# Optimization experiments

Measured on AMD Instinct MI355X. Metric: run time of the kernel, lower is better.

Reference implementation:

```python
import jax, jax.numpy as jnp
import numpy as np
from jax import lax

EPS = 1e-5


def _bn(x, gamma, beta, mean, var):
    # x: [B,C,H,W]; params: [C]
    inv = gamma / jnp.sqrt(var + EPS)
    return x * inv[None, :, None, None] + (beta - mean * inv)[None, :, None, None]


def _conv1x1(x, w):
    # w: [O, C] pointwise conv
    return jnp.einsum('oc,bchw->bohw', w, x)


def setup_inputs() -> dict:
    dim, num_heads = 256, 8
    B, H, W = 4, 40, 40
    key = jax.random.key(0)
    ks = jax.random.split(key, 12)
    inp = {
        'x': jax.random.normal(ks[0], (B, dim, H, W), jnp.float32),
        # qkv: Conv(dim, 2*dim, k=1) = conv1x1 (no bias) + BN + SiLU
        'qkv_w': jax.random.normal(ks[1], (2 * dim, dim), jnp.float32) * 0.05,
        'qkv_gamma': jax.random.uniform(ks[2], (2 * dim,), jnp.float32, 0.5, 1.5),
        'qkv_beta': jax.random.normal(ks[3], (2 * dim,), jnp.float32) * 0.05,
        'qkv_mean': jax.random.normal(ks[4], (2 * dim,), jnp.float32) * 0.05,
        'qkv_var': jax.random.uniform(ks[5], (2 * dim,), jnp.float32, 0.5, 1.5),
        # proj: Conv(dim, dim, k=1)
        'proj_w': jax.random.normal(ks[6], (dim, dim), jnp.float32) * 0.05,
        'proj_gamma': jax.random.uniform(ks[7], (dim,), jnp.float32, 0.5, 1.5),
        'proj_beta': jax.random.normal(ks[8], (dim,), jnp.float32) * 0.05,
        'proj_mean': jax.random.normal(ks[9], (dim,), jnp.float32) * 0.05,
        'proj_var': jax.random.uniform(ks[10], (dim,), jnp.float32, 0.5, 1.5),
        # pe: depthwise 3x3 conv (groups=dim, no bias) + BN (no activation)
        'pe_w': jax.random.normal(ks[11], (dim, 1, 3, 3), jnp.float32) * 0.1,
        'pe_gamma': jax.random.uniform(jax.random.fold_in(key, 100), (dim,), jnp.float32, 0.5, 1.5),
        'pe_beta': jax.random.normal(jax.random.fold_in(key, 101), (dim,), jnp.float32) * 0.05,
        'pe_mean': jax.random.normal(jax.random.fold_in(key, 102), (dim,), jnp.float32) * 0.05,
        'pe_var': jax.random.uniform(jax.random.fold_in(key, 103), (dim,), jnp.float32, 0.5, 1.5),
    }
    return inp


def reference(x, qkv_w, qkv_gamma, qkv_beta, qkv_mean, qkv_var,
              proj_w, proj_gamma, proj_beta, proj_mean, proj_var,
              pe_w, pe_gamma, pe_beta, pe_mean, pe_var):
    B, C, H, W = x.shape
    num_heads = 8
    head_dim = C // num_heads
    N = H * W

    # positional encoding: depthwise 3x3 conv + BN
    pe = lax.conv_general_dilated(
        x, pe_w, window_strides=(1, 1), padding='SAME',
        feature_group_count=C, dimension_numbers=('NCHW', 'OIHW', 'NCHW'))
    pe = _bn(pe, pe_gamma, pe_beta, pe_mean, pe_var)

    # qkv: 1x1 conv + BN + SiLU, then split into q, k along channels
    qkv = jax.nn.silu(_bn(_conv1x1(x, qkv_w), qkv_gamma, qkv_beta, qkv_mean, qkv_var))
    q, k = qkv[:, :C], qkv[:, C:]
    v = x + pe

    # reshape to heads: q,v -> [B,h,N,d]; k -> [B,h,d,N]
    q = q.reshape(B, num_heads, head_dim, N).transpose(0, 1, 3, 2)
    k = k.reshape(B, num_heads, head_dim, N)
    v = v.reshape(B, num_heads, head_dim, N).transpose(0, 1, 3, 2)

    scale = head_dim ** (-0.5)
    attn = jnp.einsum('bhnd,bhdm->bhnm', q, k) * scale  # [B,h,N,N]
    attn = jax.nn.softmax(attn, axis=-1)
    out = jnp.einsum('bhnm,bhmd->bhnd', attn, v)        # [B,h,N,d]
    out = out.transpose(0, 1, 3, 2).reshape(B, C, H, W)

    # proj: 1x1 conv + BN + SiLU
    return jax.nn.silu(_bn(_conv1x1(out, proj_w), proj_gamma, proj_beta, proj_mean, proj_var))
```

## Files before the change

kernel.cpp:

```cpp
#include <hip/hip_runtime.h>
#include <hip/hip_bf16.h>

typedef __attribute__((ext_vector_type(8))) short short8;
typedef __attribute__((ext_vector_type(4))) float f32x4;

__device__ __forceinline__ unsigned short f2bf(float f){
    union { float f; unsigned u; } uf; uf.f = f;
    unsigned u = uf.u;
    u += 0x7FFFu + ((u >> 16) & 1u);
    return (unsigned short)(u >> 16);
}
__device__ __forceinline__ int pack2(float a, float b){
    union { float f; unsigned u; } ua, ub; ua.f = a; ub.f = b;
    unsigned x = ua.u; x += 0x7FFFu + ((x >> 16) & 1u);
    unsigned y = ub.u; y += 0x7FFFu + ((y >> 16) & 1u);
    return (int)((x >> 16) | (y & 0xFFFF0000u));
}
__device__ __forceinline__ unsigned cvtpk(float lo, float hi){
    unsigned r;
    asm("v_cvt_pk_bf16_f32 %0, %1, %2" : "=v"(r) : "v"(lo), "v"(hi));
    return r;
}
__device__ __forceinline__ float fexp2(float x){
    return __builtin_amdgcn_exp2f(x);
}
__device__ __forceinline__ void load_lds16(const void* g, void* l){
    __builtin_amdgcn_global_load_lds(
        (const __attribute__((address_space(1))) unsigned int*)g,
        (__attribute__((address_space(3))) unsigned int*)l,
        16, 0, 0);
}

#define N_SPATIAL 1600
#define QSCALE_LOG2E 0.25506601f
#define LSTR 40

__global__ __launch_bounds__(256) void k_head(const float* __restrict__ x,
                                              const float* __restrict__ pw,
                                              const float* __restrict__ pg,
                                              const float* __restrict__ pb,
                                              const float* __restrict__ pm,
                                              const float* __restrict__ pv,
                                              unsigned short* __restrict__ x_t,
                                              unsigned short* __restrict__ v_mf){
    __shared__ float xs[32][163];
    int bi = blockIdx.x;
    int t = threadIdx.x;
    if (bi < 200){
        int b = bi / 50, nc = bi % 50;
        int n0 = nc * 32;
        int c = t;
        unsigned short vals[32];
        const float* src = x + ((size_t)(b*256 + c))*N_SPATIAL + n0;
        #pragma unroll
        for (int j=0;j<8;j++){
            float4 f = *reinterpret_cast<const float4*>(src + j*4);
            vals[j*4+0] = f2bf(f.x); vals[j*4+1] = f2bf(f.y);
            vals[j*4+2] = f2bf(f.z); vals[j*4+3] = f2bf(f.w);
        }
        unsigned short* dst = x_t + ((size_t)b*N_SPATIAL + n0)*256 + c;
        #pragma unroll
        for (int j=0;j<32;j++) dst[(size_t)j*256] = vals[j];
        return;
    }
    int pbi = bi - 200;
    int b = pbi/200, h=(pbi/25)%8, kt=pbi%25;
    int winStart = kt*64 - 48;
    const float* xbase = x + ((size_t)(b*256 + h*32))*N_SPATIAL;
    #pragma unroll
    for (int i=0;i<20;i++){
        int idx = t + i*256;
        int row = idx / 160, col = idx - row*160;
        int n = winStart + col;
        float val = ((unsigned)n < 1600u) ? xbase[(size_t)row*N_SPATIAL + n] : 0.f;
        xs[row][col] = val;
    }
    __syncthreads();

    int f = t>>6, lane = t&63, ql = lane&15, lg = lane>>4;
    int d = (f>>1)*16 + ql;
    int c = h*32 + d;
    float inv = pg[c]*rsqrtf(pv[c]+1e-5f);
    float bias = pb[c]-pm[c]*inv;
    const float* w9 = pw + c*9;
    float w00=w9[0],w01=w9[1],w02=w9[2],w10=w9[3],w11=w9[4],w12=w9[5],w20=w9[6],w21=w9[7],w22=w9[8];
    const float* xr = xs[d];
    union { unsigned short u[8]; int4 i4; } vals;
    #pragma unroll
    for (int j=0;j<8;j++){
        int key = (f&1)*32 + (j>>2)*16 + 4*lg + (j&3);
        int n = kt*64 + key;
        int hh = n/40, ww = n - hh*40;
        int col = key + 48;
        float acc = 0.f;
        if (hh > 0){
            if (ww > 0)  acc += xr[col-41]*w00;
                         acc += xr[col-40]*w01;
            if (ww < 39) acc += xr[col-39]*w02;
        }
        if (ww > 0)  acc += xr[col-1]*w10;
                     acc += xr[col]*w11;
        if (ww < 39) acc += xr[col+1]*w12;
        if (hh < 39){
            if (ww > 0)  acc += xr[col+39]*w20;
                         acc += xr[col+40]*w21;
            if (ww < 39) acc += xr[col+41]*w22;
        }
        float out = xr[col] + acc*inv + bias;
        vals.u[j] = f2bf(out);
    }
    *reinterpret_cast<int4*>(v_mf + ((size_t)(pbi*4 + f)*64 + lane)*8) = vals.i4;
}

__global__ __launch_bounds__(256) void k_qkv2(const unsigned short* __restrict__ x_t,
                                              const float* __restrict__ wq,
                                              const float* __restrict__ g,
                                              const float* __restrict__ be,
                                              const float* __restrict__ mu,
                                              const float* __restrict__ va,
                                              unsigned short* __restrict__ q_t,
                                              unsigned short* __restrict__ k_mf){
    __shared__ alignas(16) unsigned short a_lds[64*LSTR];
    __shared__ alignas(16) unsigned short b_lds[64*LSTR];
    int bi = blockIdx.x;
    int b = bi / 200, ot = (bi/25) % 8, nt = bi % 25;
    int o0 = ot*64, n0 = nt*64;
    int tid = threadIdx.x, w = tid>>6, lane = tid&63;
    int row = tid>>2, col8 = (tid&3)*8;
    int ql = lane&15, lg = lane>>4;
    f32x4 acc[4];
    #pragma unroll
    for (int t=0;t<4;t++) acc[t] = (f32x4){0.f,0.f,0.f,0.f};
    const float* asrc = wq + (size_t)(o0+row)*256 + col8;
    const unsigned short* bsrc = x_t + ((size_t)b*N_SPATIAL + n0 + row)*256 + col8;
    for (int k0=0; k0<256; k0+=32){
        float4 f0 = *reinterpret_cast<const float4*>(asrc + k0);
        float4 f1 = *reinterpret_cast<const float4*>(asrc + k0 + 4);
        int4 av; av.x = pack2(f0.x,f0.y); av.y = pack2(f0.z,f0.w);
                 av.z = pack2(f1.x,f1.y); av.w = pack2(f1.z,f1.w);
        *reinterpret_cast<int4*>(&a_lds[row*LSTR + col8]) = av;
        *reinterpret_cast<int4*>(&b_lds[row*LSTR + col8]) = *reinterpret_cast<const int4*>(bsrc + k0);
        __syncthreads();
        short8 af = *reinterpret_cast<const short8*>(&a_lds[(16*w + ql)*LSTR + lg*8]);
        #pragma unroll
        for (int t=0;t<4;t++){
            short8 bf = *reinterpret_cast<const short8*>(&b_lds[(16*t + ql)*LSTR + lg*8]);
            acc[t] = __builtin_amdgcn_mfma_f32_16x16x32_bf16(af, bf, acc[t], 0, 0, 0);
        }
        __syncthreads();
    }
    int ob = o0 + 16*w + 4*lg;
    int d0 = ob & 31;
    float invr[4], b2r[4];
    #pragma unroll
    for (int r=0;r<4;r++){
        int o = ob + r;
        invr[r] = g[o] * rsqrtf(va[o] + 1e-5f);
        b2r[r]  = be[o] - mu[o]*invr[r];
    }
    if (ob < 256){
        int grp = ob >> 5;
        unsigned short* dstb = q_t + ((size_t)(b*8 + grp)*N_SPATIAL)*32 + d0;
        #pragma unroll
        for (int t=0;t<4;t++){
            int n = n0 + 16*t + ql;
            float y[4];
            #pragma unroll
            for (int r=0;r<4;r++){
                float z = acc[t][r]*invr[r] + b2r[r];
                y[r] = (z / (1.f + __expf(-z))) * QSCALE_LOG2E;
            }
            *reinterpret_cast<uint2*>(dstb + (size_t)n*32) =
                make_uint2((unsigned)pack2(y[0],y[1]), (unsigned)pack2(y[2],y[3]));
        }
    } else {
        int hh = (ob>>5) - 8;
        size_t kbase = (size_t)((b*8+hh)*25)*2048;
        #pragma unroll
        for (int t=0;t<4;t++){
            int n = n0 + 16*t + ql;
            int kt = n>>6, tf = (n>>4)&3, qr = n&15;
            float y[4];
            #pragma unroll
            for (int r=0;r<4;r++){
                float z = acc[t][r]*invr[r] + b2r[r];
                y[r] = z / (1.f + __expf(-z));
            }
            size_t off = kbase + (size_t)kt*2048 + tf*512 + ((d0>>3)*16 + qr)*8 + (d0&7);
            *reinterpret_cast<uint2*>(k_mf + off) =
                make_uint2((unsigned)pack2(y[0],y[1]), (unsigned)pack2(y[2],y[3]));
        }
    }
}

__global__ __launch_bounds__(256) void k_attn8(const unsigned short* __restrict__ q_t,
                                               const unsigned short* __restrict__ k_mf,
                                               const unsigned short* __restrict__ v_mf,
                                               unsigned short* __restrict__ ao_t){
    __shared__ alignas(16) unsigned short k_lds[4][2048];
    __shared__ alignas(16) unsigned short v_lds[4][2048];
    int l = blockIdx.x;
    int xc = l & 7, j = l >> 3;
    int gg = xc + 8*(j/25);
    int b = gg >> 3, h = gg & 7, qt = j % 25;
    int tid = threadIdx.x, w = tid>>6, lane = tid&63;
    int ql = lane&15, lg = lane>>4;
    int nq = qt*64 + w*16 + ql;

    const unsigned short* qsrc = q_t + ((size_t)(b*8+h)*N_SPATIAL)*32;
    const unsigned short* kms  = k_mf + (size_t)((b*8+h)*25)*2048;
    const unsigned short* vms  = v_mf + (size_t)(b*200 + h*25)*2048;

    short8 qf = *reinterpret_cast<const short8*>(qsrc + (size_t)nq*32 + lg*8);

    const unsigned short* kg = kms + w*512 + lane*8;
    const unsigned short* vg = vms + w*512 + lane*8;

    load_lds16(kg,        &k_lds[0][w*512]);
    load_lds16(vg,        &v_lds[0][w*512]);
    load_lds16(kg + 2048, &k_lds[1][w*512]);
    load_lds16(vg + 2048, &v_lds[1][w*512]);

    f32x4 o0 = (f32x4){0.f,0.f,0.f,0.f};
    f32x4 o1 = (f32x4){0.f,0.f,0.f,0.f};
    float Sp = 0.f;

    for (int kt = 0; kt < 25; ++kt){
        if (kt+2 < 25){
            int bidx = (kt+2)&3;
            load_lds16(kg + (size_t)(kt+2)*2048, &k_lds[bidx][w*512]);
            load_lds16(vg + (size_t)(kt+2)*2048, &v_lds[bidx][w*512]);
        }
        if (kt < 23)       asm volatile("s_waitcnt vmcnt(4)" ::: "memory");
        else if (kt == 23) asm volatile("s_waitcnt vmcnt(2)" ::: "memory");
        else               asm volatile("s_waitcnt vmcnt(0)" ::: "memory");
        __builtin_amdgcn_s_barrier();
        asm volatile("" ::: "memory");

        const unsigned short* kb = &k_lds[kt&3][0];
        const unsigned short* vb = &v_lds[kt&3][0];
        short8 ka0 = *reinterpret_cast<const short8*>(kb +    0 + lane*8);
        short8 ka1 = *reinterpret_cast<const short8*>(kb +  512 + lane*8);
        short8 ka2 = *reinterpret_cast<const short8*>(kb + 1024 + lane*8);
        short8 ka3 = *reinterpret_cast<const short8*>(kb + 1536 + lane*8);

        f32x4 z = (f32x4){0.f,0.f,0.f,0.f};
        f32x4 p0 = __builtin_amdgcn_mfma_f32_16x16x32_bf16(ka0, qf, z, 0,0,0);
        f32x4 p1 = __builtin_amdgcn_mfma_f32_16x16x32_bf16(ka1, qf, z, 0,0,0);
        f32x4 p2 = __builtin_amdgcn_mfma_f32_16x16x32_bf16(ka2, qf, z, 0,0,0);
        f32x4 p3 = __builtin_amdgcn_mfma_f32_16x16x32_bf16(ka3, qf, z, 0,0,0);

        #pragma unroll
        for (int r=0;r<4;r++){
            p0[r] = fexp2(p0[r]);
            p1[r] = fexp2(p1[r]);
            p2[r] = fexp2(p2[r]);
            p3[r] = fexp2(p3[r]);
        }
        Sp += ((p0[0]+p0[1])+(p0[2]+p0[3])) + ((p1[0]+p1[1])+(p1[2]+p1[3]))
            + ((p2[0]+p2[1])+(p2[2]+p2[3])) + ((p3[0]+p3[1])+(p3[2]+p3[3]));

        union { int4 i; short8 s8; } pb0, pb1;
        pb0.i = make_int4((int)cvtpk(p0[0],p0[1]), (int)cvtpk(p0[2],p0[3]),
                          (int)cvtpk(p1[0],p1[1]), (int)cvtpk(p1[2],p1[3]));
        pb1.i = make_int4((int)cvtpk(p2[0],p2[1]), (int)cvtpk(p2[2],p2[3]),
                          (int)cvtpk(p3[0],p3[1]), (int)cvtpk(p3[2],p3[3]));

        short8 va0 = *reinterpret_cast<const short8*>(vb +    0 + lane*8);
        short8 va1 = *reinterpret_cast<const short8*>(vb +  512 + lane*8);
        short8 va2 = *reinterpret_cast<const short8*>(vb + 1024 + lane*8);
        short8 va3 = *reinterpret_cast<const short8*>(vb + 1536 + lane*8);

        o0 = __builtin_amdgcn_mfma_f32_16x16x32_bf16(va0, pb0.s8, o0, 0,0,0);
        o0 = __builtin_amdgcn_mfma_f32_16x16x32_bf16(va1, pb1.s8, o0, 0,0,0);
        o1 = __builtin_amdgcn_mfma_f32_16x16x32_bf16(va2, pb0.s8, o1, 0,0,0);
        o1 = __builtin_amdgcn_mfma_f32_16x16x32_bf16(va3, pb1.s8, o1, 0,0,0);
    }

    Sp += __shfl_xor(Sp, 16);
    Sp += __shfl_xor(Sp, 32);
    float inv = 1.f / Sp;
    size_t rowoff = ((size_t)b*N_SPATIAL + nq)*256 + h*32;
    uint2 w0 = make_uint2((unsigned)pack2(o0[0]*inv, o0[1]*inv),
                          (unsigned)pack2(o0[2]*inv, o0[3]*inv));
    *reinterpret_cast<uint2*>(ao_t + rowoff + 4*lg) = w0;
    uint2 w1 = make_uint2((unsigned)pack2(o1[0]*inv, o1[1]*inv),
                          (unsigned)pack2(o1[2]*inv, o1[3]*inv));
    *reinterpret_cast<uint2*>(ao_t + rowoff + 16 + 4*lg) = w1;
}

__global__ __launch_bounds__(256) void k_proj2(const unsigned short* __restrict__ ao_t,
                                               const float* __restrict__ wp,
                                               const float* __restrict__ g,
                                               const float* __restrict__ be,
                                               const float* __restrict__ mu,
                                               const float* __restrict__ va,
                                               float* __restrict__ out){
    __shared__ alignas(16) unsigned short a_lds[64*LSTR];
    __shared__ alignas(16) unsigned short b_lds[64*LSTR];
    int bi = blockIdx.x;
    int b = bi / 100, ot = (bi/25) % 4, nt = bi % 25;
    int o0 = ot*64, n0 = nt*64;
    int tid = threadIdx.x, w = tid>>6, lane = tid&63;
    int row = tid>>2, col8 = (tid&3)*8;
    int ql = lane&15, lg = lane>>4;
    f32x4 acc[4];
    #pragma unroll
    for (int t=0;t<4;t++) acc[t] = (f32x4){0.f,0.f,0.f,0.f};
    const float* asrc = wp + (size_t)(o0+row)*256 + col8;
    const unsigned short* bsrc = ao_t + ((size_t)b*N_SPATIAL + n0 + row)*256 + col8;
    for (int k0=0; k0<256; k0+=32){
        float4 f0 = *reinterpret_cast<const float4*>(asrc + k0);
        float4 f1 = *reinterpret_cast<const float4*>(asrc + k0 + 4);
        int4 av; av.x = pack2(f0.x,f0.y); av.y = pack2(f0.z,f0.w);
                 av.z = pack2(f1.x,f1.y); av.w = pack2(f1.z,f1.w);
        *reinterpret_cast<int4*>(&a_lds[row*LSTR + col8]) = av;
        *reinterpret_cast<int4*>(&b_lds[row*LSTR + col8]) = *reinterpret_cast<const int4*>(bsrc + k0);
        __syncthreads();
        short8 af = *reinterpret_cast<const short8*>(&a_lds[(16*w + ql)*LSTR + lg*8]);
        #pragma unroll
        for (int t=0;t<4;t++){
            short8 bf = *reinterpret_cast<const short8*>(&b_lds[(16*t + ql)*LSTR + lg*8]);
            acc[t] = __builtin_amdgcn_mfma_f32_16x16x32_bf16(af, bf, acc[t], 0, 0, 0);
        }
        __syncthreads();
    }
    #pragma unroll
    for (int r=0;r<4;r++){
        int o = o0 + 16*w + lg*4 + r;
        float inv = g[o] * rsqrtf(va[o] + 1e-5f);
        float b2  = be[o] - mu[o]*inv;
        float* dst = out + ((size_t)(b*256 + o))*N_SPATIAL;
        #pragma unroll
        for (int t=0;t<4;t++){
            int n = n0 + 16*t + ql;
            float z = acc[t][r]*inv + b2;
            float y = z / (1.f + __expf(-z));
            dst[n] = y;
        }
    }
}

extern "C" void kernel_launch(void* const* d_in, const int* in_sizes, int n_in,
                              void* d_out, int out_size, void* d_ws, size_t ws_size,
                              hipStream_t stream) {
    const float* x      = (const float*)d_in[0];
    const float* qkv_w  = (const float*)d_in[1];
    const float* qkv_g  = (const float*)d_in[2];
    const float* qkv_b  = (const float*)d_in[3];
    const float* qkv_m  = (const float*)d_in[4];
    const float* qkv_v  = (const float*)d_in[5];
    const float* proj_w = (const float*)d_in[6];
    const float* proj_g = (const float*)d_in[7];
    const float* proj_b = (const float*)d_in[8];
    const float* proj_m = (const float*)d_in[9];
    const float* proj_v = (const float*)d_in[10];
    const float* pe_w   = (const float*)d_in[11];
    const float* pe_g   = (const float*)d_in[12];
    const float* pe_b   = (const float*)d_in[13];
    const float* pe_m   = (const float*)d_in[14];
    const float* pe_v   = (const float*)d_in[15];

    char* ws = (char*)d_ws;
    unsigned short* x_t  = (unsigned short*)(ws);
    unsigned short* v_mf = (unsigned short*)(ws + 3276800);
    unsigned short* q_t  = (unsigned short*)(ws + 6553600);
    unsigned short* k_mf = (unsigned short*)(ws + 9830400);
    unsigned short* ao_t = (unsigned short*)(ws + 13107200);
    float* outp = (float*)d_out;

    k_head <<<1000,256, 0, stream>>>(x, pe_w, pe_g, pe_b, pe_m, pe_v, x_t, v_mf);
    k_qkv2 <<<800, 256, 0, stream>>>(x_t, qkv_w, qkv_g, qkv_b, qkv_m, qkv_v, q_t, k_mf);
    k_attn8<<<800, 256, 0, stream>>>(q_t, k_mf, v_mf, ao_t);
    k_proj2<<<400, 256, 0, stream>>>(ao_t, proj_w, proj_g, proj_b, proj_m, proj_v, outp);
}
```

Before: 62.21 us.

## Split attention keys across two waves, fuse x transpose into head, shrink proj tiles

The attention kernel now uses 128-thread blocks. Each wave handles all 64 queries of a tile (four Q fragments) over half of the key tiles, double-buffering K and V into per-wave LDS. The two partial results and row sums are merged through LDS at the end. The x-to-bf16 transpose is folded into the depthwise-conv head blocks so they reuse x data already staged in LDS, removing 200 separate blocks. The projection GEMM uses 32-column tiles to double the grid to 800 blocks. The trade-offs are more registers per wave in attention, fewer waves per block, and an extra cross-wave combine step.

```diff
diff --git a/kernel.cpp b/kernel.cpp
--- a/kernel.cpp
+++ b/kernel.cpp
@@ -35,36 +35,18 @@
 #define QSCALE_LOG2E 0.25506601f
 #define LSTR 40
 
-__global__ __launch_bounds__(256) void k_head(const float* __restrict__ x,
-                                              const float* __restrict__ pw,
-                                              const float* __restrict__ pg,
-                                              const float* __restrict__ pb,
-                                              const float* __restrict__ pm,
-                                              const float* __restrict__ pv,
-                                              unsigned short* __restrict__ x_t,
-                                              unsigned short* __restrict__ v_mf){
+__global__ __launch_bounds__(256) void k_head2(const float* __restrict__ x,
+                                               const float* __restrict__ pw,
+                                               const float* __restrict__ pg,
+                                               const float* __restrict__ pb,
+                                               const float* __restrict__ pm,
+                                               const float* __restrict__ pv,
+                                               unsigned short* __restrict__ x_t,
+                                               unsigned short* __restrict__ v_mf){
     __shared__ float xs[32][163];
-    int bi = blockIdx.x;
+    int pbi = blockIdx.x;
+    int b = pbi/200, h=(pbi/25)%8, kt=pbi%25;
     int t = threadIdx.x;
-    if (bi < 200){
-        int b = bi / 50, nc = bi % 50;
-        int n0 = nc * 32;
-        int c = t;
-        unsigned short vals[32];
-        const float* src = x + ((size_t)(b*256 + c))*N_SPATIAL + n0;
-        #pragma unroll
-        for (int j=0;j<8;j++){
-            float4 f = *reinterpret_cast<const float4*>(src + j*4);
-            vals[j*4+0] = f2bf(f.x); vals[j*4+1] = f2bf(f.y);
-            vals[j*4+2] = f2bf(f.z); vals[j*4+3] = f2bf(f.w);
-        }
-        unsigned short* dst = x_t + ((size_t)b*N_SPATIAL + n0)*256 + c;
-        #pragma unroll
-        for (int j=0;j<32;j++) dst[(size_t)j*256] = vals[j];
-        return;
-    }
-    int pbi = bi - 200;
-    int b = pbi/200, h=(pbi/25)%8, kt=pbi%25;
     int winStart = kt*64 - 48;
     const float* xbase = x + ((size_t)(b*256 + h*32))*N_SPATIAL;
     #pragma unroll
@@ -76,6 +58,16 @@
         xs[row][col] = val;
     }
     __syncthreads();
+
+    {
+        unsigned short* xtb = x_t + ((size_t)b*N_SPATIAL + kt*64)*256 + h*32;
+        #pragma unroll
+        for (int i=0;i<8;i++){
+            int idx = t + i*256;
+            int cl = idx & 31, nl = idx >> 5;
+            xtb[(size_t)nl*256 + cl] = f2bf(xs[cl][nl + 48]);
+        }
+    }
 
     int f = t>>6, lane = t&63, ql = lane&15, lg = lane>>4;
     int d = (f>>1)*16 + ql;
@@ -193,103 +185,149 @@
     }
 }
 
-__global__ __launch_bounds__(256) void k_attn8(const unsigned short* __restrict__ q_t,
-                                               const unsigned short* __restrict__ k_mf,
-                                               const unsigned short* __restrict__ v_mf,
-                                               unsigned short* __restrict__ ao_t){
-    __shared__ alignas(16) unsigned short k_lds[4][2048];
-    __shared__ alignas(16) unsigned short v_lds[4][2048];
+__global__ __launch_bounds__(128) void k_attn10(const unsigned short* __restrict__ q_t,
+                                                const unsigned short* __restrict__ k_mf,
+                                                const unsigned short* __restrict__ v_mf,
+                                                unsigned short* __restrict__ ao_t){
+    __shared__ alignas(16) unsigned short lds_all[2][2][2][2048];
     int l = blockIdx.x;
     int xc = l & 7, j = l >> 3;
     int gg = xc + 8*(j/25);
     int b = gg >> 3, h = gg & 7, qt = j % 25;
     int tid = threadIdx.x, w = tid>>6, lane = tid&63;
     int ql = lane&15, lg = lane>>4;
-    int nq = qt*64 + w*16 + ql;
 
     const unsigned short* qsrc = q_t + ((size_t)(b*8+h)*N_SPATIAL)*32;
-    const unsigned short* kms  = k_mf + (size_t)((b*8+h)*25)*2048;
-    const unsigned short* vms  = v_mf + (size_t)(b*200 + h*25)*2048;
-
-    short8 qf = *reinterpret_cast<const short8*>(qsrc + (size_t)nq*32 + lg*8);
-
-    const unsigned short* kg = kms + w*512 + lane*8;
-    const unsigned short* vg = vms + w*512 + lane*8;
-
-    load_lds16(kg,        &k_lds[0][w*512]);
-    load_lds16(vg,        &v_lds[0][w*512]);
-    load_lds16(kg + 2048, &k_lds[1][w*512]);
-    load_lds16(vg + 2048, &v_lds[1][w*512]);
-
-    f32x4 o0 = (f32x4){0.f,0.f,0.f,0.f};
-    f32x4 o1 = (f32x4){0.f,0.f,0.f,0.f};
-    float Sp = 0.f;
-
-    for (int kt = 0; kt < 25; ++kt){
-        if (kt+2 < 25){
-            int bidx = (kt+2)&3;
-            load_lds16(kg + (size_t)(kt+2)*2048, &k_lds[bidx][w*512]);
-            load_lds16(vg + (size_t)(kt+2)*2048, &v_lds[bidx][w*512]);
-        }
-        if (kt < 23)       asm volatile("s_waitcnt vmcnt(4)" ::: "memory");
-        else if (kt == 23) asm volatile("s_waitcnt vmcnt(2)" ::: "memory");
-        else               asm volatile("s_waitcnt vmcnt(0)" ::: "memory");
-        __builtin_amdgcn_s_barrier();
-        asm volatile("" ::: "memory");
-
-        const unsigned short* kb = &k_lds[kt&3][0];
-        const unsigned short* vb = &v_lds[kt&3][0];
-        short8 ka0 = *reinterpret_cast<const short8*>(kb +    0 + lane*8);
-        short8 ka1 = *reinterpret_cast<const short8*>(kb +  512 + lane*8);
-        short8 ka2 = *reinterpret_cast<const short8*>(kb + 1024 + lane*8);
-        short8 ka3 = *reinterpret_cast<const short8*>(kb + 1536 + lane*8);
-
-        f32x4 z = (f32x4){0.f,0.f,0.f,0.f};
-        f32x4 p0 = __builtin_amdgcn_mfma_f32_16x16x32_bf16(ka0, qf, z, 0,0,0);
-        f32x4 p1 = __builtin_amdgcn_mfma_f32_16x16x32_bf16(ka1, qf, z, 0,0,0);
-        f32x4 p2 = __builtin_amdgcn_mfma_f32_16x16x32_bf16(ka2, qf, z, 0,0,0);
-        f32x4 p3 = __builtin_amdgcn_mfma_f32_16x16x32_bf16(ka3, qf, z, 0,0,0);
-
-        #pragma unroll
-        for (int r=0;r<4;r++){
-            p0[r] = fexp2(p0[r]);
-            p1[r] = fexp2(p1[r]);
-            p2[r] = fexp2(p2[r]);
-            p3[r] = fexp2(p3[r]);
-        }
-        Sp += ((p0[0]+p0[1])+(p0[2]+p0[3])) + ((p1[0]+p1[1])+(p1[2]+p1[3]))
-            + ((p2[0]+p2[1])+(p2[2]+p2[3])) + ((p3[0]+p3[1])+(p3[2]+p3[3]));
-
-        union { int4 i; short8 s8; } pb0, pb1;
-        pb0.i = make_int4((int)cvtpk(p0[0],p0[1]), (int)cvtpk(p0[2],p0[3]),
-                          (int)cvtpk(p1[0],p1[1]), (int)cvtpk(p1[2],p1[3]));
-        pb1.i = make_int4((int)cvtpk(p2[0],p2[1]), (int)cvtpk(p2[2],p2[3]),
-                          (int)cvtpk(p3[0],p3[1]), (int)cvtpk(p3[2],p3[3]));
-
-        short8 va0 = *reinterpret_cast<const short8*>(vb +    0 + lane*8);
-        short8 va1 = *reinterpret_cast<const short8*>(vb +  512 + lane*8);
-        short8 va2 = *reinterpret_cast<const short8*>(vb + 1024 + lane*8);
-        short8 va3 = *reinterpret_cast<const short8*>(vb + 1536 + lane*8);
-
-        o0 = __builtin_amdgcn_mfma_f32_16x16x32_bf16(va0, pb0.s8, o0, 0,0,0);
-        o0 = __builtin_amdgcn_mfma_f32_16x16x32_bf16(va1, pb1.s8, o0, 0,0,0);
-        o1 = __builtin_amdgcn_mfma_f32_16x16x32_bf16(va2, pb0.s8, o1, 0,0,0);
-        o1 = __builtin_amdgcn_mfma_f32_16x16x32_bf16(va3, pb1.s8, o1, 0,0,0);
-    }
-
-    Sp += __shfl_xor(Sp, 16);
-    Sp += __shfl_xor(Sp, 32);
-    float inv = 1.f / Sp;
-    size_t rowoff = ((size_t)b*N_SPATIAL + nq)*256 + h*32;
-    uint2 w0 = make_uint2((unsigned)pack2(o0[0]*inv, o0[1]*inv),
-                          (unsigned)pack2(o0[2]*inv, o0[3]*inv));
-    *reinterpret_cast<uint2*>(ao_t + rowoff + 4*lg) = w0;
-    uint2 w1 = make_uint2((unsigned)pack2(o1[0]*inv, o1[1]*inv),
-                          (unsigned)pack2(o1[2]*inv, o1[3]*inv));
-    *reinterpret_cast<uint2*>(ao_t + rowoff + 16 + 4*lg) = w1;
-}
-
-__global__ __launch_bounds__(256) void k_proj2(const unsigned short* __restrict__ ao_t,
+    const unsigned short* kms  = k_mf + (size_t)((b*8+h)*25)*2048 + lane*8;
+    const unsigned short* vms  = v_mf + (size_t)(b*200 + h*25)*2048 + lane*8;
+
+    short8 qf[4];
+    #pragma unroll
+    for (int qj=0;qj<4;qj++)
+        qf[qj] = *reinterpret_cast<const short8*>(qsrc + (size_t)(qt*64 + qj*16 + ql)*32 + lg*8);
+
+    f32x4 acc[2][4];
+    #pragma unroll
+    for (int di=0;di<2;di++)
+        #pragma unroll
+        for (int qj=0;qj<4;qj++) acc[di][qj] = (f32x4){0.f,0.f,0.f,0.f};
+    float Sp[4] = {0.f,0.f,0.f,0.f};
+
+    int t0 = w ? 13 : 0, t1 = w ? 25 : 13;
+    unsigned short* kb0 = &lds_all[w][0][0][0];
+    unsigned short* vb0 = &lds_all[w][0][1][0];
+    unsigned short* kb1 = &lds_all[w][1][0][0];
+    unsigned short* vb1 = &lds_all[w][1][1][0];
+
+    {
+        const unsigned short* ks = kms + (size_t)t0*2048;
+        const unsigned short* vs = vms + (size_t)t0*2048;
+        load_lds16(ks,        kb0);
+        load_lds16(ks +  512, kb0 +  512);
+        load_lds16(ks + 1024, kb0 + 1024);
+        load_lds16(ks + 1536, kb0 + 1536);
+        load_lds16(vs,        vb0);
+        load_lds16(vs +  512, vb0 +  512);
+        load_lds16(vs + 1024, vb0 + 1024);
+        load_lds16(vs + 1536, vb0 + 1536);
+    }
+
+    for (int i = t0; i < t1; ++i){
+        int cb = (i - t0) & 1;
+        unsigned short* kb = cb ? kb1 : kb0;
+        unsigned short* vb = cb ? vb1 : vb0;
+        if (i+1 < t1){
+            unsigned short* kn = cb ? kb0 : kb1;
+            unsigned short* vn = cb ? vb0 : vb1;
+            const unsigned short* ks = kms + (size_t)(i+1)*2048;
+            const unsigned short* vs = vms + (size_t)(i+1)*2048;
+            load_lds16(ks,        kn);
+            load_lds16(ks +  512, kn +  512);
+            load_lds16(ks + 1024, kn + 1024);
+            load_lds16(ks + 1536, kn + 1536);
+            load_lds16(vs,        vn);
+            load_lds16(vs +  512, vn +  512);
+            load_lds16(vs + 1024, vn + 1024);
+            load_lds16(vs + 1536, vn + 1536);
+            asm volatile("s_waitcnt vmcnt(8)" ::: "memory");
+        } else {
+            asm volatile("s_waitcnt vmcnt(0)" ::: "memory");
+        }
+        __builtin_amdgcn_sched_barrier(0);
+
+        #pragma unroll
+        for (int half=0; half<2; ++half){
+            short8 kfa = *reinterpret_cast<const short8*>(kb + (2*half  )*512 + lane*8);
+            short8 kfb = *reinterpret_cast<const short8*>(kb + (2*half+1)*512 + lane*8);
+            short8 vfa = *reinterpret_cast<const short8*>(vb + (half    )*512 + lane*8);
+            short8 vfb = *reinterpret_cast<const short8*>(vb + (2+half  )*512 + lane*8);
+            #pragma unroll
+            for (int qj=0;qj<4;qj++){
+                f32x4 z = (f32x4){0.f,0.f,0.f,0.f};
+                f32x4 p0 = __builtin_amdgcn_mfma_f32_16x16x32_bf16(kfa, qf[qj], z, 0,0,0);
+                f32x4 p1 = __builtin_amdgcn_mfma_f32_16x16x32_bf16(kfb, qf[qj], z, 0,0,0);
+                #pragma unroll
+                for (int r=0;r<4;r++){
+                    p0[r] = fexp2(p0[r]);
+                    p1[r] = fexp2(p1[r]);
+                }
+                Sp[qj] += ((p0[0]+p0[1])+(p0[2]+p0[3])) + ((p1[0]+p1[1])+(p1[2]+p1[3]));
+                union { int4 i4; short8 s8; } pb;
+                pb.i4 = make_int4((int)cvtpk(p0[0],p0[1]), (int)cvtpk(p0[2],p0[3]),
+                                  (int)cvtpk(p1[0],p1[1]), (int)cvtpk(p1[2],p1[3]));
+                acc[0][qj] = __builtin_amdgcn_mfma_f32_16x16x32_bf16(vfa, pb.s8, acc[0][qj], 0,0,0);
+                acc[1][qj] = __builtin_amdgcn_mfma_f32_16x16x32_bf16(vfb, pb.s8, acc[1][qj], 0,0,0);
+            }
+        }
+    }
+
+    float* cmb = (float*)&lds_all[1][0][0][0];
+    __syncthreads();
+    if (w == 1){
+        float* p = cmb + lane*36;
+        #pragma unroll
+        for (int di=0;di<2;di++)
+            #pragma unroll
+            for (int qj=0;qj<4;qj++)
+                #pragma unroll
+                for (int r=0;r<4;r++) p[(di*4+qj)*4+r] = acc[di][qj][r];
+        #pragma unroll
+        for (int qj=0;qj<4;qj++) p[32+qj] = Sp[qj];
+    }
+    __syncthreads();
+    if (w == 0){
+        const float* p = cmb + lane*36;
+        #pragma unroll
+        for (int di=0;di<2;di++)
+            #pragma unroll
+            for (int qj=0;qj<4;qj++)
+                #pragma unroll
+                for (int r=0;r<4;r++) acc[di][qj][r] += p[(di*4+qj)*4+r];
+        float invq[4];
+        #pragma unroll
+        for (int qj=0;qj<4;qj++){
+            float s = Sp[qj] + p[32+qj];
+            s += __shfl_xor(s, 16);
+            s += __shfl_xor(s, 32);
+            invq[qj] = 1.f / s;
+        }
+        size_t rowbase = ((size_t)b*N_SPATIAL + qt*64)*256 + h*32;
+        #pragma unroll
+        for (int qj=0;qj<4;qj++){
+            size_t ro = rowbase + (size_t)(qj*16 + ql)*256 + 4*lg;
+            float iv = invq[qj];
+            #pragma unroll
+            for (int di=0;di<2;di++){
+                uint2 wv = make_uint2(
+                    (unsigned)pack2(acc[di][qj][0]*iv, acc[di][qj][1]*iv),
+                    (unsigned)pack2(acc[di][qj][2]*iv, acc[di][qj][3]*iv));
+                *reinterpret_cast<uint2*>(ao_t + ro + di*16) = wv;
+            }
+        }
+    }
+}
+
+__global__ __launch_bounds__(256) void k_proj4(const unsigned short* __restrict__ ao_t,
                                                const float* __restrict__ wp,
                                                const float* __restrict__ g,
                                                const float* __restrict__ be,
@@ -297,29 +335,30 @@
                                                const float* __restrict__ va,
                                                float* __restrict__ out){
     __shared__ alignas(16) unsigned short a_lds[64*LSTR];
-    __shared__ alignas(16) unsigned short b_lds[64*LSTR];
+    __shared__ alignas(16) unsigned short b_lds[32*LSTR];
     int bi = blockIdx.x;
-    int b = bi / 100, ot = (bi/25) % 4, nt = bi % 25;
-    int o0 = ot*64, n0 = nt*64;
+    int b = bi / 200, ot = (bi/50) % 4, nt = bi % 50;
+    int o0 = ot*64, n0 = nt*32;
     int tid = threadIdx.x, w = tid>>6, lane = tid&63;
-    int row = tid>>2, col8 = (tid&3)*8;
+    int arow = tid>>2, acol8 = (tid&3)*8;
+    int brow = tid>>3, bcol4 = (tid&7)*4;
     int ql = lane&15, lg = lane>>4;
-    f32x4 acc[4];
-    #pragma unroll
-    for (int t=0;t<4;t++) acc[t] = (f32x4){0.f,0.f,0.f,0.f};
-    const float* asrc = wp + (size_t)(o0+row)*256 + col8;
-    const unsigned short* bsrc = ao_t + ((size_t)b*N_SPATIAL + n0 + row)*256 + col8;
+    f32x4 acc[2];
+    acc[0] = (f32x4){0.f,0.f,0.f,0.f};
+    acc[1] = (f32x4){0.f,0.f,0.f,0.f};
+    const float* asrc = wp + (size_t)(o0+arow)*256 + acol8;
+    const unsigned short* bsrc = ao_t + ((size_t)b*N_SPATIAL + n0 + brow)*256 + bcol4;
     for (int k0=0; k0<256; k0+=32){
         float4 f0 = *reinterpret_cast<const float4*>(asrc + k0);
         float4 f1 = *reinterpret_cast<const float4*>(asrc + k0 + 4);
         int4 av; av.x = pack2(f0.x,f0.y); av.y = pack2(f0.z,f0.w);
                  av.z = pack2(f1.x,f1.y); av.w = pack2(f1.z,f1.w);
-        *reinterpret_cast<int4*>(&a_lds[row*LSTR + col8]) = av;
-        *reinterpret_cast<int4*>(&b_lds[row*LSTR + col8]) = *reinterpret_cast<const int4*>(bsrc + k0);
+        *reinterpret_cast<int4*>(&a_lds[arow*LSTR + acol8]) = av;
+        *reinterpret_cast<uint2*>(&b_lds[brow*LSTR + bcol4]) = *reinterpret_cast<const uint2*>(bsrc + k0);
         __syncthreads();
         short8 af = *reinterpret_cast<const short8*>(&a_lds[(16*w + ql)*LSTR + lg*8]);
         #pragma unroll
-        for (int t=0;t<4;t++){
+        for (int t=0;t<2;t++){
             short8 bf = *reinterpret_cast<const short8*>(&b_lds[(16*t + ql)*LSTR + lg*8]);
             acc[t] = __builtin_amdgcn_mfma_f32_16x16x32_bf16(af, bf, acc[t], 0, 0, 0);
         }
@@ -332,7 +371,7 @@
         float b2  = be[o] - mu[o]*inv;
         float* dst = out + ((size_t)(b*256 + o))*N_SPATIAL;
         #pragma unroll
-        for (int t=0;t<4;t++){
+        for (int t=0;t<2;t++){
             int n = n0 + 16*t + ql;
             float z = acc[t][r]*inv + b2;
             float y = z / (1.f + __expf(-z));
@@ -369,8 +408,8 @@
     unsigned short* ao_t = (unsigned short*)(ws + 13107200);
     float* outp = (float*)d_out;
 
-    k_head <<<1000,256, 0, stream>>>(x, pe_w, pe_g, pe_b, pe_m, pe_v, x_t, v_mf);
-    k_qkv2 <<<800, 256, 0, stream>>>(x_t, qkv_w, qkv_g, qkv_b, qkv_m, qkv_v, q_t, k_mf);
-    k_attn8<<<800, 256, 0, stream>>>(q_t, k_mf, v_mf, ao_t);
-    k_proj2<<<400, 256, 0, stream>>>(ao_t, proj_w, proj_g, proj_b, proj_m, proj_v, outp);
-}
+    k_head2 <<<800, 256, 0, stream>>>(x, pe_w, pe_g, pe_b, pe_m, pe_v, x_t, v_mf);
+    k_qkv2  <<<800, 256, 0, stream>>>(x_t, qkv_w, qkv_g, qkv_b, qkv_m, qkv_v, q_t, k_mf);
+    k_attn10<<<800, 128, 0, stream>>>(q_t, k_mf, v_mf, ao_t);
+    k_proj4 <<<800, 256, 0, stream>>>(ao_t, proj_w, proj_g, proj_b, proj_m, proj_v, outp);
+}
```

Measured after the change: 61.58 us. About the same (-1.0%).
